# Kernel optimization log

Hardware: AMD Instinct MI355X
Metric: run time of the kernel (lower is better)

Reference implementation:

```python
import jax, jax.numpy as jnp
import numpy as np
from jax import lax

B, HS, WS, C, NH, WIN = 32, 56, 56, 192, 6, 7
HID = int(C * 4.0)
EPS = 1e-5


def _ln(x, g, b):
    m = jnp.mean(x, -1, keepdims=True)
    v = jnp.mean((x - m) ** 2, -1, keepdims=True)
    return (x - m) * jax.lax.rsqrt(v + EPS) * g + b


def _cpe(x, H, W, w, b):
    # x: [B, H*W, C]; depthwise 3x3 conv positional encoding, residual add
    Bn = x.shape[0]
    feat = x.reshape(Bn, H, W, C).transpose(0, 3, 1, 2)  # NCHW
    out = lax.conv_general_dilated(feat, w, (1, 1), 'SAME',
                                   feature_group_count=C,
                                   dimension_numbers=('NCHW', 'OIHW', 'NCHW'))
    out = out + b[None, :, None, None]
    pos = out.transpose(0, 2, 3, 1).reshape(Bn, H * W, C)
    return x + pos


def _window_attn(xw, qkv_w, qkv_b, proj_w, proj_b):
    # xw: [nW, N, C]; faithful einops split 'b n (d k h) -> k b h n d'
    nW, N, _ = xw.shape
    hd = C // NH
    qkv = xw @ qkv_w + qkv_b                      # [nW, N, 3C]
    qkv = qkv.reshape(nW, N, hd, 3, NH)           # (d k h) split
    q, k, v = jnp.moveaxis(qkv.transpose(3, 0, 4, 1, 2), 0, 0)  # each [nW, NH, N, hd]
    scale = hd ** -0.5
    scores = jnp.einsum('bhid,bhjd->bhij', q, k) * scale
    attn = jax.nn.softmax(scores, axis=-1)
    out = jnp.einsum('bhij,bhjd->bhid', attn, v)  # [nW, NH, N, hd]
    out = out.transpose(0, 2, 1, 3).reshape(nW, N, C)  # 'b h n d -> b n (h d)'
    return out @ proj_w + proj_b


def _forward(x, H, W, cpe0_w, cpe0_b, cpe1_w, cpe1_b, n1_g, n1_b,
             qkv_w, qkv_b, proj_w, proj_b, n2_g, n2_b,
             fc1_w, fc1_b, fc2_w, fc2_b):
    Bn = x.shape[0]
    shortcut = _cpe(x, H, W, cpe0_w, cpe0_b)
    y = _ln(shortcut, n1_g, n1_b).reshape(Bn, H, W, C)
    pad_r = (WIN - W % WIN) % WIN
    pad_b = (WIN - H % WIN) % WIN
    y = jnp.pad(y, ((0, 0), (0, pad_b), (0, pad_r), (0, 0)))
    Hp, Wp = H + pad_b, W + pad_r
    nh, nw = Hp // WIN, Wp // WIN
    # faithful: 'b (w_h nw_h) (w_w nw_w) c -> (b nw_h nw_w) (w_h w_w) c'
    y = y.reshape(Bn, WIN, nh, WIN, nw, C).transpose(0, 2, 4, 1, 3, 5)
    y = y.reshape(Bn * nh * nw, WIN * WIN, C)
    y = _window_attn(y, qkv_w, qkv_b, proj_w, proj_b)
    # reverse: '(b nw_h nw_w) (w_h w_w) c -> b (w_h nw_h) (w_w nw_w) c'
    y = y.reshape(Bn, nh, nw, WIN, WIN, C).transpose(0, 3, 1, 4, 2, 5)
    y = y.reshape(Bn, Hp, Wp, C)[:, :H, :W, :].reshape(Bn, H * W, C)
    y = shortcut + y
    y = _cpe(y, H, W, cpe1_w, cpe1_b)
    h = _ln(y, n2_g, n2_b)
    h = jax.nn.gelu(h @ fc1_w + fc1_b, approximate=False) @ fc2_w + fc2_b
    return y + h


def setup_inputs() -> dict:
    key = jax.random.key(0)
    ks = jax.random.split(key, 12)
    s = 0.02
    return {
        'x': jax.random.normal(ks[0], (B, HS * WS, C), jnp.float32),
        'H': HS, 'W': WS,
        'cpe0_w': jax.random.normal(ks[1], (C, 1, 3, 3), jnp.float32) * s,
        'cpe0_b': jnp.zeros((C,), jnp.float32),
        'cpe1_w': jax.random.normal(ks[2], (C, 1, 3, 3), jnp.float32) * s,
        'cpe1_b': jnp.zeros((C,), jnp.float32),
        'n1_g': jnp.ones((C,), jnp.float32), 'n1_b': jnp.zeros((C,), jnp.float32),
        'qkv_w': jax.random.normal(ks[3], (C, 3 * C), jnp.float32) * s,
        'qkv_b': jnp.zeros((3 * C,), jnp.float32),
        'proj_w': jax.random.normal(ks[4], (C, C), jnp.float32) * s,
        'proj_b': jnp.zeros((C,), jnp.float32),
        'n2_g': jnp.ones((C,), jnp.float32), 'n2_b': jnp.zeros((C,), jnp.float32),
        'fc1_w': jax.random.normal(ks[5], (C, HID), jnp.float32) * s,
        'fc1_b': jnp.zeros((HID,), jnp.float32),
        'fc2_w': jax.random.normal(ks[6], (HID, C), jnp.float32) * s,
        'fc2_b': jnp.zeros((C,), jnp.float32),
    }


def reference(x, H, W, cpe0_w, cpe0_b, cpe1_w, cpe1_b, n1_g, n1_b,
              qkv_w, qkv_b, proj_w, proj_b, n2_g, n2_b,
              fc1_w, fc1_b, fc2_w, fc2_b):
    return _forward(x, H, W, cpe0_w, cpe0_b, cpe1_w, cpe1_b, n1_g, n1_b,
                    qkv_w, qkv_b, proj_w, proj_b, n2_g, n2_b,
                    fc1_w, fc1_b, fc2_w, fc2_b)
```

## Files before the change

kernel.cpp:

```cpp
#include <hip/hip_runtime.h>
#include <hip/hip_bf16.h>
#include <math.h>

#define Bn   32
#define Hh   56
#define Wd   56
#define Cc   192
#define NHh  6
#define HDim 32
#define HIDN 768
#define Tt   (Bn*Hh*Wd)
#define NWIN (Bn*64)

typedef __attribute__((ext_vector_type(8))) short short8;
typedef __attribute__((ext_vector_type(4))) short s4v;
typedef __attribute__((ext_vector_type(4))) float floatx4;

__device__ __forceinline__ short f2bf(float f) {
    unsigned u = __float_as_uint(f);
    u += 0x7fffu + ((u >> 16) & 1u);
    return (short)(u >> 16);
}
__device__ __forceinline__ float bf2f(short s) {
    return __uint_as_float(((unsigned)(unsigned short)s) << 16);
}

__device__ __forceinline__ void gl_lds16(const short* g, short* l) {
    __builtin_amdgcn_global_load_lds(
        (const __attribute__((address_space(1))) unsigned int*)g,
        (__attribute__((address_space(3))) unsigned int*)l,
        16, 0, 0);
}

__device__ __forceinline__ int xcd_swz(int bid, int nb) {
    return (bid & 7) * (nb >> 3) + (bid >> 3);
}

__global__ void k_transpose(const float* __restrict__ W, short* __restrict__ WT,
                            int K, int N) {
    int idx = blockIdx.x * 256 + threadIdx.x;
    if (idx >= K * N) return;
    int n = idx / K, k = idx % K;
    WT[idx] = f2bf(W[k * N + n]);
}

__global__ void k_transpose_qkv(const float* __restrict__ W, short* __restrict__ WT) {
    int idx = blockIdx.x * 256 + threadIdx.x;
    if (idx >= 192 * 576) return;
    int n = idx / 192, kk = idx % 192;
    int d = n & 31, hh = (n >> 5) % 6, k3 = n / 192;
    int oc = d * 18 + k3 * 6 + hh;
    WT[idx] = f2bf(W[kk * 576 + oc]);
}

template<int ADDP>
__global__ void __launch_bounds__(256) k_cpe_ln(
    const float* __restrict__ xin, const float* __restrict__ wconv,
    const float* __restrict__ bconv, const float* __restrict__ g,
    const float* __restrict__ beta, float* __restrict__ ysum_out,
    short* __restrict__ ln_out, int windowed, const short* __restrict__ proj)
{
    const int lane = threadIdx.x & 63;
    const int wv   = threadIdx.x >> 6;
    const bool act = lane < 48;
    const int c4   = (lane < 48 ? lane : lane - 16) * 4;

    const floatx4 zf = {0.f, 0.f, 0.f, 0.f};
    float wreg[36];
    #pragma unroll
    for (int i = 0; i < 9; ++i)
        *(floatx4*)&wreg[i * 4] = *(const floatx4*)(wconv + c4 * 9 + i * 4);
    const floatx4 gv  = *(const floatx4*)(g + c4);
    const floatx4 bv  = *(const floatx4*)(beta + c4);
    const floatx4 bcv = *(const floatx4*)(bconv + c4);

    const int W = xcd_swz(blockIdx.x, gridDim.x) * 4 + wv;
    const int b = W / (Hh * 7);
    const int rem = W % (Hh * 7);
    const int h = rem / 7, wslot = rem % 7;
    const int w0 = wslot * 8;

    floatx4 r[3][10];
    const int hy0 = (h > 0) ? h - 1 : 0;
    const int hy2 = (h < Hh - 1) ? h + 1 : Hh - 1;
    const int hys[3] = {hy0, h, hy2};
    #pragma unroll
    for (int dy = 0; dy < 3; ++dy) {
        const int hy = hys[dy];
        const float* rp = xin + ((size_t)b * (Hh * Wd) + hy * Wd) * Cc + c4;
        #pragma unroll
        for (int j = 0; j < 10; ++j) {
            int wx = w0 - 1 + j;
            int wc = (wx < 0) ? 0 : ((wx > Wd - 1) ? Wd - 1 : wx);
            floatx4 v = *(const floatx4*)(rp + wc * Cc);
            if (ADDP) {
                int prow = (b * 64 + (hy & 7) * 8 + (wc & 7)) * 49
                         + (hy >> 3) * 7 + (wc >> 3);
                s4v pv = *(const s4v*)(proj + (size_t)prow * Cc + c4);
                #pragma unroll
                for (int q = 0; q < 4; ++q) v[q] += bf2f(pv[q]);
            }
            r[dy][j] = v;
        }
    }
    if (h == 0) {
        #pragma unroll
        for (int j = 0; j < 10; ++j) r[0][j] = zf;
    }
    if (h == Hh - 1) {
        #pragma unroll
        for (int j = 0; j < 10; ++j) r[2][j] = zf;
    }
    if (w0 == 0)      { r[0][0] = zf; r[1][0] = zf; r[2][0] = zf; }
    if (w0 == Wd - 8) { r[0][9] = zf; r[1][9] = zf; r[2][9] = zf; }

    floatx4 val[8];
    #pragma unroll
    for (int tk = 0; tk < 8; ++tk) {
        floatx4 a = bcv;
        #pragma unroll
        for (int dy = 0; dy < 3; ++dy) {
            #pragma unroll
            for (int dx = 0; dx < 3; ++dx) {
                const int t = dy * 3 + dx;
                floatx4 v = r[dy][tk + dx];
                #pragma unroll
                for (int j = 0; j < 4; ++j)
                    a[j] += wreg[j * 9 + t] * v[j];
            }
        }
        floatx4 xc = r[1][tk + 1];
        #pragma unroll
        for (int j = 0; j < 4; ++j) val[tk][j] = xc[j] + a[j];
    }

    float s[8], s2[8];
    #pragma unroll
    for (int tk = 0; tk < 8; ++tk) {
        float a = val[tk][0] + val[tk][1] + val[tk][2] + val[tk][3];
        float a2 = val[tk][0]*val[tk][0] + val[tk][1]*val[tk][1]
                 + val[tk][2]*val[tk][2] + val[tk][3]*val[tk][3];
        s[tk]  = act ? a  : 0.f;
        s2[tk] = act ? a2 : 0.f;
    }
    #pragma unroll
    for (int off = 1; off < 64; off <<= 1) {
        #pragma unroll
        for (int tk = 0; tk < 8; ++tk) {
            s[tk]  += __shfl_xor(s[tk],  off, 64);
            s2[tk] += __shfl_xor(s2[tk], off, 64);
        }
    }

    const int blk0 = (b * Hh + h) * Wd + w0;
    #pragma unroll
    for (int tk = 0; tk < 8; ++tk) {
        const float mean = s[tk] * (1.0f / Cc);
        const float var  = s2[tk] * (1.0f / Cc) - mean * mean;
        const float rs   = rsqrtf(var + 1e-5f);
        int rr;
        if (windowed) {
            int win = b * 64 + (h & 7) * 8 + tk;
            int pos = (h >> 3) * 7 + wslot;
            rr = win * 49 + pos;
        } else {
            rr = blk0 + tk;
        }
        if (act) {
            *(floatx4*)(ysum_out + (size_t)(blk0 + tk) * Cc + c4) = val[tk];
            s4v o;
            #pragma unroll
            for (int j = 0; j < 4; ++j)
                o[j] = f2bf((val[tk][j] - mean) * rs * gv[j] + bv[j]);
            *(s4v*)(ln_out + (size_t)rr * Cc + c4) = o;
        }
    }
}

template<int K, int EPI>
__global__ void __launch_bounds__(256) k_gemm_tiled(
    const short* __restrict__ A, const short* __restrict__ BT,
    const float* __restrict__ bias, void* __restrict__ outp)
{
    __shared__ __align__(16) short As[2][128 * 32];
    __shared__ __align__(16) short Bs[2][64 * 32];
    const int tid = threadIdx.x;
    const int gx = gridDim.x;
    const int flat = blockIdx.y * gx + blockIdx.x;
    const int swz = xcd_swz(flat, gx * gridDim.y);
    const int n0 = (swz % gx) * 64;
    const int m0 = (swz / gx) * 128;
    const int w = tid >> 6, lane = tid & 63;
    const int lcol = lane & 15, quad = lane >> 4;

    floatx4 acc[2][4];
    #pragma unroll
    for (int mi = 0; mi < 2; ++mi)
        #pragma unroll
        for (int ni = 0; ni < 4; ++ni) acc[mi][ni] = (floatx4){0, 0, 0, 0};

    const int ar = tid >> 2, ac = (tid & 3) * 8;
    const short* agp  = A + (size_t)(m0 + ar) * K + ac;
    const short* agp2 = A + (size_t)(m0 + 64 + ar) * K + ac;
    const short* bgp  = BT + (size_t)(n0 + ar) * K + ac;

    const int aoff = w * 32 + lcol;

    gl_lds16(agp, &As[0][tid * 8]);
    gl_lds16(agp2, &As[0][64 * 32 + tid * 8]);
    gl_lds16(bgp, &Bs[0][tid * 8]);

    #pragma unroll 2
    for (int t = 0; t < K / 32; ++t) {
        const int b = t & 1;
        __syncthreads();
        if (t + 1 < K / 32) {
            const int k1 = (t + 1) * 32;
            gl_lds16(agp + k1, &As[b ^ 1][tid * 8]);
            gl_lds16(agp2 + k1, &As[b ^ 1][64 * 32 + tid * 8]);
            gl_lds16(bgp + k1, &Bs[b ^ 1][tid * 8]);
        }
        short8 a0 = *(const short8*)&As[b][aoff * 32 + quad * 8];
        short8 a1 = *(const short8*)&As[b][(aoff + 16) * 32 + quad * 8];
        #pragma unroll
        for (int ni = 0; ni < 4; ++ni) {
            short8 bb = *(const short8*)&Bs[b][(ni * 16 + lcol) * 32 + quad * 8];
            acc[0][ni] = __builtin_amdgcn_mfma_f32_16x16x32_bf16(a0, bb, acc[0][ni], 0, 0, 0);
            acc[1][ni] = __builtin_amdgcn_mfma_f32_16x16x32_bf16(a1, bb, acc[1][ni], 0, 0, 0);
        }
    }

    #pragma unroll
    for (int mi = 0; mi < 2; ++mi) {
        #pragma unroll
        for (int ni = 0; ni < 4; ++ni) {
            int col = n0 + ni * 16 + lcol;
            float bv;
            if (EPI == 0) {
                int d = col & 31, hh = (col >> 5) % 6, k3 = col / 192;
                bv = bias[d * 18 + k3 * 6 + hh];
            } else {
                bv = bias[col];
            }
            #pragma unroll
            for (int t = 0; t < 4; ++t) {
                int row = m0 + w * 32 + mi * 16 + quad * 4 + t;
                float v = acc[mi][ni][t] + bv;
                if (EPI == 0) {
                    ((short*)outp)[(size_t)row * 576 + col] = f2bf(v);
                } else if (EPI == 2) {
                    float gl = 0.5f * v * (1.0f + erff(v * 0.70710678118654752f));
                    ((short*)outp)[(size_t)row * HIDN + col] = f2bf(gl);
                } else if (EPI == 3) {
                    ((float*)outp)[(size_t)row * Cc + col] += v;
                } else {
                    ((short*)outp)[(size_t)row * Cc + col] = f2bf(v);
                }
            }
        }
    }
}

__global__ void __launch_bounds__(64) k_attn(
    const short* __restrict__ C, short* __restrict__ aout)
{
    int h = blockIdx.x, win = blockIdx.y;
    int lane = threadIdx.x;
    int lcol = lane & 15, quad = lane >> 4;
    __shared__ __align__(16) short buf[7424];
    short* Q  = buf;
    short* Kb = buf + 2560;
    short* Vt = buf + 5120;
    short* P  = buf;

    const short8 z8 = {0, 0, 0, 0, 0, 0, 0, 0};
    const size_t wbase = (size_t)win * 49 * 576;
    const int hq = h * 32;
    const int pr = lane >> 2, d8 = (lane & 3) * 8;

    #pragma unroll
    for (int it = 0; it < 4; ++it) {
        int pp = pr + it * 16;
        bool ok = pp < 49;
        size_t ro = wbase + (size_t)(ok ? pp : 0) * 576 + hq + d8;
        short8 vq = ok ? *(const short8*)(C + ro)       : z8;
        short8 vk = ok ? *(const short8*)(C + ro + 192) : z8;
        *(short8*)(Q  + pp * 40 + d8) = vq;
        *(short8*)(Kb + pp * 40 + d8) = vk;
    }
    #pragma unroll
    for (int it = 0; it < 4; ++it) {
        int pp = pr + it * 16;
        bool ok = pp < 49;
        size_t ro = wbase + (size_t)(ok ? pp : 0) * 576 + 384 + hq + d8;
        short8 vv = ok ? *(const short8*)(C + ro) : z8;
        #pragma unroll
        for (int j = 0; j < 8; ++j)
            Vt[(d8 + j) * 72 + pp] = vv[j];
    }

    floatx4 s[4][4];
    #pragma unroll
    for (int mi = 0; mi < 4; ++mi) {
        short8 aq = *(const short8*)(Q + (mi * 16 + lcol) * 40 + quad * 8);
        #pragma unroll
        for (int ni = 0; ni < 4; ++ni) {
            short8 bk = *(const short8*)(Kb + (ni * 16 + lcol) * 40 + quad * 8);
            floatx4 z = {0, 0, 0, 0};
            s[mi][ni] = __builtin_amdgcn_mfma_f32_16x16x32_bf16(aq, bk, z, 0, 0, 0);
        }
    }

    const float scale = 0.17677669529663688f;
    #pragma unroll
    for (int mi = 0; mi < 4; ++mi) {
        #pragma unroll
        for (int reg = 0; reg < 4; ++reg) {
            float vv[4];
            float mx = -3e38f;
            #pragma unroll
            for (int ni = 0; ni < 4; ++ni) {
                int col = ni * 16 + lcol;
                float v = (col < 49) ? s[mi][ni][reg] * scale : -3e38f;
                vv[ni] = v;
                mx = fmaxf(mx, v);
            }
            #pragma unroll
            for (int off = 1; off < 16; off <<= 1)
                mx = fmaxf(mx, __shfl_xor(mx, off, 64));
            float sum = 0.f;
            #pragma unroll
            for (int ni = 0; ni < 4; ++ni) {
                int col = ni * 16 + lcol;
                float e = (col < 49) ? __expf(vv[ni] - mx) : 0.f;
                vv[ni] = e;
                sum += e;
            }
            #pragma unroll
            for (int off = 1; off < 16; off <<= 1)
                sum += __shfl_xor(sum, off, 64);
            float inv = 1.0f / sum;
            int row = mi * 16 + quad * 4 + reg;
            #pragma unroll
            for (int ni = 0; ni < 4; ++ni)
                P[row * 72 + ni * 16 + lcol] = f2bf(vv[ni] * inv);
        }
    }

    #pragma unroll
    for (int mi = 0; mi < 4; ++mi) {
        short8 a0 = *(const short8*)(P + (mi * 16 + lcol) * 72 + quad * 8);
        short8 a1 = *(const short8*)(P + (mi * 16 + lcol) * 72 + 32 + quad * 8);
        #pragma unroll
        for (int nd = 0; nd < 2; ++nd) {
            short8 b0 = *(const short8*)(Vt + (nd * 16 + lcol) * 72 + quad * 8);
            short8 b1 = *(const short8*)(Vt + (nd * 16 + lcol) * 72 + 32 + quad * 8);
            floatx4 z = {0, 0, 0, 0};
            floatx4 o = __builtin_amdgcn_mfma_f32_16x16x32_bf16(a0, b0, z, 0, 0, 0);
            o = __builtin_amdgcn_mfma_f32_16x16x32_bf16(a1, b1, o, 0, 0, 0);
            #pragma unroll
            for (int reg = 0; reg < 4; ++reg) {
                int row = mi * 16 + quad * 4 + reg;
                if (row < 49)
                    aout[((size_t)win * 49 + row) * Cc + h * HDim + nd * 16 + lcol] =
                        f2bf(o[reg]);
            }
        }
    }
}

extern "C" void kernel_launch(void* const* d_in, const int* in_sizes, int n_in,
                              void* d_out, int out_size, void* d_ws, size_t ws_size,
                              hipStream_t stream)
{
    (void)in_sizes; (void)n_in; (void)out_size; (void)ws_size;
    const float* x      = (const float*)d_in[0];
    const float* cpe0_w = (const float*)d_in[3];
    const float* cpe0_b = (const float*)d_in[4];
    const float* cpe1_w = (const float*)d_in[5];
    const float* cpe1_b = (const float*)d_in[6];
    const float* n1_g   = (const float*)d_in[7];
    const float* n1_b   = (const float*)d_in[8];
    const float* qkv_w  = (const float*)d_in[9];
    const float* qkv_b  = (const float*)d_in[10];
    const float* proj_w = (const float*)d_in[11];
    const float* proj_b = (const float*)d_in[12];
    const float* n2_g   = (const float*)d_in[13];
    const float* n2_b   = (const float*)d_in[14];
    const float* fc1_w  = (const float*)d_in[15];
    const float* fc1_b  = (const float*)d_in[16];
    const float* fc2_w  = (const float*)d_in[17];
    const float* fc2_b  = (const float*)d_in[18];
    float* out = (float*)d_out;

    char* ws = (char*)d_ws;
    float* shortcut = (float*)ws;
    short* lnbuf    = (short*)(ws + 77070336);
    short* qkvbuf   = (short*)(ws + 115605504);
    short* attnout  = (short*)(ws + 231211008);
    short* projbuf  = qkvbuf;
    short* h1       = qkvbuf;
    short* wqkvT    = (short*)(ws + 269746176);
    short* wprojT   = (short*)(ws + 269967360);
    short* wfc1T    = (short*)(ws + 270041088);
    short* wfc2T    = (short*)(ws + 270336000);

    k_transpose_qkv<<<dim3((192 * 576 + 255) / 256), dim3(256), 0, stream>>>(qkv_w, wqkvT);
    k_transpose<<<dim3((192 * 192 + 255) / 256), dim3(256), 0, stream>>>(proj_w, wprojT, 192, 192);
    k_transpose<<<dim3((192 * 768 + 255) / 256), dim3(256), 0, stream>>>(fc1_w, wfc1T, 192, 768);
    k_transpose<<<dim3((768 * 192 + 255) / 256), dim3(256), 0, stream>>>(fc2_w, wfc2T, 768, 192);

    k_cpe_ln<0><<<dim3(Tt / 32), dim3(256), 0, stream>>>(x, cpe0_w, cpe0_b, n1_g, n1_b,
                                                         shortcut, lnbuf, 1, nullptr);
    k_gemm_tiled<192, 0><<<dim3(9, Tt / 128), dim3(256), 0, stream>>>(lnbuf, wqkvT, qkv_b, qkvbuf);
    k_attn<<<dim3(NHh, NWIN), dim3(64), 0, stream>>>(qkvbuf, attnout);
    k_gemm_tiled<192, 4><<<dim3(3, Tt / 128), dim3(256), 0, stream>>>(attnout, wprojT, proj_b, projbuf);
    k_cpe_ln<1><<<dim3(Tt / 32), dim3(256), 0, stream>>>(shortcut, cpe1_w, cpe1_b, n2_g, n2_b,
                                                         out, lnbuf, 0, projbuf);
    k_gemm_tiled<192, 2><<<dim3(12, Tt / 128), dim3(256), 0, stream>>>(lnbuf, wfc1T, fc1_b, h1);
    k_gemm_tiled<768, 3><<<dim3(3, Tt / 128), dim3(256), 0, stream>>>(h1, wfc2T, fc2_b, out);
}
```

Baseline: 560.4 us.

## Store residual intermediates in bf16 and merge weight transpose kernels

Stores the shortcut and the post-attention residual sum as bf16 instead of fp32, so the CPE/LN kernels and the final FC2 epilogue read and write half the bytes. The FC2 epilogue no longer does a read-modify-write on the fp32 output; it reads the bf16 residual from a separate buffer and writes the output once. The four weight-transpose launches are merged into one kernel. Rounding the residual stream to bf16 adds precision error to the final output.

```diff
diff --git a/kernel.cpp b/kernel.cpp
--- a/kernel.cpp
+++ b/kernel.cpp
@@ -36,30 +36,46 @@
     return (bid & 7) * (nb >> 3) + (bid >> 3);
 }
 
-__global__ void k_transpose(const float* __restrict__ W, short* __restrict__ WT,
-                            int K, int N) {
+#define NQKV (192*576)
+#define NPRJ (192*192)
+#define NFC1 (192*768)
+#define NFC2 (768*192)
+__global__ void k_transpose_all(
+    const float* __restrict__ qkv_w, const float* __restrict__ proj_w,
+    const float* __restrict__ fc1_w, const float* __restrict__ fc2_w,
+    short* __restrict__ wqkvT, short* __restrict__ wprojT,
+    short* __restrict__ wfc1T, short* __restrict__ wfc2T)
+{
     int idx = blockIdx.x * 256 + threadIdx.x;
-    if (idx >= K * N) return;
-    int n = idx / K, k = idx % K;
-    WT[idx] = f2bf(W[k * N + n]);
-}
-
-__global__ void k_transpose_qkv(const float* __restrict__ W, short* __restrict__ WT) {
-    int idx = blockIdx.x * 256 + threadIdx.x;
-    if (idx >= 192 * 576) return;
-    int n = idx / 192, kk = idx % 192;
-    int d = n & 31, hh = (n >> 5) % 6, k3 = n / 192;
-    int oc = d * 18 + k3 * 6 + hh;
-    WT[idx] = f2bf(W[kk * 576 + oc]);
+    if (idx < NQKV) {
+        int n = idx / 192, kk = idx % 192;
+        int d = n & 31, hh = (n >> 5) % 6, k3 = n / 192;
+        int oc = d * 18 + k3 * 6 + hh;
+        wqkvT[idx] = f2bf(qkv_w[kk * 576 + oc]);
+    } else if (idx < NQKV + NPRJ) {
+        int i = idx - NQKV;
+        int n = i / 192, k = i % 192;
+        wprojT[i] = f2bf(proj_w[k * 192 + n]);
+    } else if (idx < NQKV + NPRJ + NFC1) {
+        int i = idx - NQKV - NPRJ;
+        int n = i / 192, k = i % 192;
+        wfc1T[i] = f2bf(fc1_w[k * 768 + n]);
+    } else if (idx < NQKV + NPRJ + NFC1 + NFC2) {
+        int i = idx - NQKV - NPRJ - NFC1;
+        int n = i / 768, k = i % 768;
+        wfc2T[i] = f2bf(fc2_w[k * 192 + n]);
+    }
 }
 
 template<int ADDP>
 __global__ void __launch_bounds__(256) k_cpe_ln(
-    const float* __restrict__ xin, const float* __restrict__ wconv,
+    const void* __restrict__ xin_, const float* __restrict__ wconv,
     const float* __restrict__ bconv, const float* __restrict__ g,
-    const float* __restrict__ beta, float* __restrict__ ysum_out,
+    const float* __restrict__ beta, short* __restrict__ ysum_out,
     short* __restrict__ ln_out, int windowed, const short* __restrict__ proj)
 {
+    const float* xf = (const float*)xin_;
+    const short* xb = (const short*)xin_;
     const int lane = threadIdx.x & 63;
     const int wv   = threadIdx.x >> 6;
     const bool act = lane < 48;
@@ -87,18 +103,21 @@
     #pragma unroll
     for (int dy = 0; dy < 3; ++dy) {
         const int hy = hys[dy];
-        const float* rp = xin + ((size_t)b * (Hh * Wd) + hy * Wd) * Cc + c4;
+        const size_t rowbase = ((size_t)b * (Hh * Wd) + hy * Wd) * Cc + c4;
         #pragma unroll
         for (int j = 0; j < 10; ++j) {
             int wx = w0 - 1 + j;
             int wc = (wx < 0) ? 0 : ((wx > Wd - 1) ? Wd - 1 : wx);
-            floatx4 v = *(const floatx4*)(rp + wc * Cc);
+            floatx4 v;
             if (ADDP) {
+                s4v xv = *(const s4v*)(xb + rowbase + (size_t)wc * Cc);
                 int prow = (b * 64 + (hy & 7) * 8 + (wc & 7)) * 49
                          + (hy >> 3) * 7 + (wc >> 3);
                 s4v pv = *(const s4v*)(proj + (size_t)prow * Cc + c4);
                 #pragma unroll
-                for (int q = 0; q < 4; ++q) v[q] += bf2f(pv[q]);
+                for (int q = 0; q < 4; ++q) v[q] = bf2f(xv[q]) + bf2f(pv[q]);
+            } else {
+                v = *(const floatx4*)(xf + rowbase + (size_t)wc * Cc);
             }
             r[dy][j] = v;
         }
@@ -167,11 +186,13 @@
             rr = blk0 + tk;
         }
         if (act) {
-            *(floatx4*)(ysum_out + (size_t)(blk0 + tk) * Cc + c4) = val[tk];
-            s4v o;
-            #pragma unroll
-            for (int j = 0; j < 4; ++j)
-                o[j] = f2bf((val[tk][j] - mean) * rs * gv[j] + bv[j]);
+            s4v ys, o;
+            #pragma unroll
+            for (int j = 0; j < 4; ++j) {
+                ys[j] = f2bf(val[tk][j]);
+                o[j]  = f2bf((val[tk][j] - mean) * rs * gv[j] + bv[j]);
+            }
+            *(s4v*)(ysum_out + (size_t)(blk0 + tk) * Cc + c4) = ys;
             *(s4v*)(ln_out + (size_t)rr * Cc + c4) = o;
         }
     }
@@ -180,7 +201,8 @@
 template<int K, int EPI>
 __global__ void __launch_bounds__(256) k_gemm_tiled(
     const short* __restrict__ A, const short* __restrict__ BT,
-    const float* __restrict__ bias, void* __restrict__ outp)
+    const float* __restrict__ bias, void* __restrict__ outp,
+    const short* __restrict__ aux)
 {
     __shared__ __align__(16) short As[2][128 * 32];
     __shared__ __align__(16) short Bs[2][64 * 32];
@@ -252,7 +274,8 @@
                     float gl = 0.5f * v * (1.0f + erff(v * 0.70710678118654752f));
                     ((short*)outp)[(size_t)row * HIDN + col] = f2bf(gl);
                 } else if (EPI == 3) {
-                    ((float*)outp)[(size_t)row * Cc + col] += v;
+                    ((float*)outp)[(size_t)row * Cc + col] =
+                        bf2f(aux[(size_t)row * Cc + col]) + v;
                 } else {
                     ((short*)outp)[(size_t)row * Cc + col] = f2bf(v);
                 }
@@ -394,7 +417,8 @@
     float* out = (float*)d_out;
 
     char* ws = (char*)d_ws;
-    float* shortcut = (float*)ws;
+    short* shortcut = (short*)ws;
+    short* ybuf     = (short*)(ws + 38535168);
     short* lnbuf    = (short*)(ws + 77070336);
     short* qkvbuf   = (short*)(ws + 115605504);
     short* attnout  = (short*)(ws + 231211008);
@@ -405,18 +429,16 @@
     short* wfc1T    = (short*)(ws + 270041088);
     short* wfc2T    = (short*)(ws + 270336000);
 
-    k_transpose_qkv<<<dim3((192 * 576 + 255) / 256), dim3(256), 0, stream>>>(qkv_w, wqkvT);
-    k_transpose<<<dim3((192 * 192 + 255) / 256), dim3(256), 0, stream>>>(proj_w, wprojT, 192, 192);
-    k_transpose<<<dim3((192 * 768 + 255) / 256), dim3(256), 0, stream>>>(fc1_w, wfc1T, 192, 768);
-    k_transpose<<<dim3((768 * 192 + 255) / 256), dim3(256), 0, stream>>>(fc2_w, wfc2T, 768, 192);
+    k_transpose_all<<<dim3((NQKV + NPRJ + NFC1 + NFC2 + 255) / 256), dim3(256), 0, stream>>>(
+        qkv_w, proj_w, fc1_w, fc2_w, wqkvT, wprojT, wfc1T, wfc2T);
 
     k_cpe_ln<0><<<dim3(Tt / 32), dim3(256), 0, stream>>>(x, cpe0_w, cpe0_b, n1_g, n1_b,
                                                          shortcut, lnbuf, 1, nullptr);
-    k_gemm_tiled<192, 0><<<dim3(9, Tt / 128), dim3(256), 0, stream>>>(lnbuf, wqkvT, qkv_b, qkvbuf);
+    k_gemm_tiled<192, 0><<<dim3(9, Tt / 128), dim3(256), 0, stream>>>(lnbuf, wqkvT, qkv_b, qkvbuf, nullptr);
     k_attn<<<dim3(NHh, NWIN), dim3(64), 0, stream>>>(qkvbuf, attnout);
-    k_gemm_tiled<192, 4><<<dim3(3, Tt / 128), dim3(256), 0, stream>>>(attnout, wprojT, proj_b, projbuf);
+    k_gemm_tiled<192, 4><<<dim3(3, Tt / 128), dim3(256), 0, stream>>>(attnout, wprojT, proj_b, projbuf, nullptr);
     k_cpe_ln<1><<<dim3(Tt / 32), dim3(256), 0, stream>>>(shortcut, cpe1_w, cpe1_b, n2_g, n2_b,
-                                                         out, lnbuf, 0, projbuf);
-    k_gemm_tiled<192, 2><<<dim3(12, Tt / 128), dim3(256), 0, stream>>>(lnbuf, wfc1T, fc1_b, h1);
-    k_gemm_tiled<768, 3><<<dim3(3, Tt / 128), dim3(256), 0, stream>>>(h1, wfc2T, fc2_b, out);
-}
+                                                         ybuf, lnbuf, 0, projbuf);
+    k_gemm_tiled<192, 2><<<dim3(12, Tt / 128), dim3(256), 0, stream>>>(lnbuf, wfc1T, fc1_b, h1, nullptr);
+    k_gemm_tiled<768, 3><<<dim3(3, Tt / 128), dim3(256), 0, stream>>>(h1, wfc2T, fc2_b, out, ybuf);
+}
```

Result: faster. 539.2 us (-3.8%).
